# Kernel tuning notes

Measured on AMD Instinct MI355X. Metric: run time of the kernel, lower is better.

Reference implementation:

```python
import jax, jax.numpy as jnp
import numpy as np
from math import sqrt

ALPHA = 1.0
EPS = 1e-8


def setup_inputs() -> dict:
    key = jax.random.key(0)
    k1, k2, k3 = jax.random.split(key, 3)
    B, L, S, H, E = 4, 2048, 2048, 16, 64
    queries = jax.random.normal(k1, (B, L, H, E), dtype=jnp.float32)
    keys = jax.random.normal(k2, (B, S, H, E), dtype=jnp.float32)
    values = jax.random.normal(k3, (B, S, H, E), dtype=jnp.float32)
    return {"queries": queries, "keys": keys, "values": values}


def reference(queries, keys, values):
    B, L, H, E = queries.shape
    scale = 1.0 / sqrt(E)
    # dot product scores: [B,H,L,S]
    dot = jnp.einsum('blhe,bshe->bhls', queries, keys)
    # squared norms: [B,H,L,1] and [B,H,1,S]
    qn2 = jnp.sum(queries * queries, axis=-1).transpose(0, 2, 1)[..., :, None]
    kn2 = jnp.sum(keys * keys, axis=-1).transpose(0, 2, 1)[..., None, :]
    # wedge (parallelogram area) norm^2 = |q|^2|k|^2 - (q.k)^2, clipped at 0
    wedge_norm = jnp.sqrt(jax.nn.relu(qn2 * kn2 - dot * dot) + EPS)
    scores = ((1.0 - ALPHA) * dot + ALPHA * wedge_norm) * scale
    A = jax.nn.softmax(scores, axis=-1)  # no mask (mask_flag=False), dropout=0
    V = jnp.einsum('bhls,bshd->blhd', A, values)
    return V, jnp.mean(jnp.abs(scores))
```

## Files before the change

### kernel.cpp

```cpp
#include <hip/hip_runtime.h>
#include <math.h>

constexpr int Bb = 4, Ll = 2048, Ss = 2048, Hh = 16, Ee = 64;
constexpr float S2E  = 0.125f * 1.44269504088896341f;
constexpr float EPS2 = 1e-8f * S2E * S2E;
constexpr float INV_CNT = 1.0f / (4.0f * 16.0f * 2048.0f * 2048.0f);
constexpr float SUM_SCALE = INV_CNT * 0.69314718055994531f;

typedef __attribute__((ext_vector_type(8))) short  short8;
typedef __attribute__((ext_vector_type(4))) float  floatx4;

#define MFMA __builtin_amdgcn_mfma_f32_16x16x32_bf16

#define GLL(gp, lp_)                                                       \
  __builtin_amdgcn_global_load_lds(                                        \
      (const __attribute__((address_space(1))) unsigned int*)(gp),         \
      (__attribute__((address_space(3))) unsigned int*)(lp_), 16, 0, 0)

__device__ __forceinline__ unsigned bfrnd(float f) {
  unsigned u = __builtin_bit_cast(unsigned, f);
  return u + 0x7fffu + ((u >> 16) & 1u);
}
__device__ __forceinline__ float sq4(float4 v) {
  return v.x * v.x + v.y * v.y + v.z * v.z + v.w * v.w;
}
__device__ __forceinline__ float4 mul4(float4 v, float s) {
  float4 r; r.x = v.x * s; r.y = v.y * s; r.z = v.z * s; r.w = v.w * s;
  return r;
}
__device__ __forceinline__ short8 pack8(float4 x, float4 y) {
  union { short8 s; unsigned u[4]; } r;
  r.u[0] = __builtin_amdgcn_perm(bfrnd(x.y), bfrnd(x.x), 0x07060302u);
  r.u[1] = __builtin_amdgcn_perm(bfrnd(x.w), bfrnd(x.z), 0x07060302u);
  r.u[2] = __builtin_amdgcn_perm(bfrnd(y.y), bfrnd(y.x), 0x07060302u);
  r.u[3] = __builtin_amdgcn_perm(bfrnd(y.w), bfrnd(y.z), 0x07060302u);
  return r.s;
}

__global__ __launch_bounds__(256) void geom_pre_kernel(
    const float* __restrict__ Kg, const float* __restrict__ Vg,
    short* __restrict__ Kbf, short* __restrict__ Vtg,
    float* __restrict__ kn2g, float* __restrict__ sumg) {
  const int tid = threadIdx.x, bid = blockIdx.x;
  const int st = bid & 31, h = (bid >> 5) & 15, b = bid >> 9;
  const int s0 = st * 64, bh = b * 16 + h;
  if (bid == 0 && tid == 0) *sumg = 0.0f;

  const int r64 = tid >> 2, ec = (tid & 3) * 16;
  const float4* kp = (const float4*)(Kg + (((size_t)b * Ss + s0 + r64) * Hh + h) * Ee + ec);
  float4 k0 = kp[0], k1 = kp[1], k2 = kp[2], k3 = kp[3];
  float kn = sq4(k0) + sq4(k1) + sq4(k2) + sq4(k3);
  kn += __shfl_xor(kn, 1);
  kn += __shfl_xor(kn, 2);
  if ((tid & 3) == 0) kn2g[(size_t)bh * Ss + s0 + r64] = kn;
  short* ko = Kbf + ((size_t)bh * Ss + s0 + r64) * Ee + ec;
  *(short8*)(ko)     = pack8(k0, k1);
  *(short8*)(ko + 8) = pack8(k2, k3);

  const int sq = tid >> 4, eq = tid & 15;
  const float* vb = Vg + (((size_t)b * Ss + s0 + sq * 4) * Hh + h) * Ee + eq * 4;
  float4 r0 = *(const float4*)(vb);
  float4 r1 = *(const float4*)(vb + Hh * Ee);
  float4 r2 = *(const float4*)(vb + 2 * Hh * Ee);
  float4 r3 = *(const float4*)(vb + 3 * Hh * Ee);
  short* vo = Vtg + ((size_t)bh * Ee + eq * 4) * Ss + s0 + sq * 4;
#pragma unroll
  for (int j = 0; j < 4; ++j) {
    uint2 t;
    t.x = __builtin_amdgcn_perm(bfrnd((&r1.x)[j]), bfrnd((&r0.x)[j]), 0x07060302u);
    t.y = __builtin_amdgcn_perm(bfrnd((&r3.x)[j]), bfrnd((&r2.x)[j]), 0x07060302u);
    *(uint2*)(vo + (size_t)j * Ss) = t;
  }
}

constexpr int KB0 = 0, VB0 = 8192, PB = 16384, KN2 = 24576;

__global__ __launch_bounds__(256, 4) void geom_attn_kernel(
    const float* __restrict__ Qg, const short* __restrict__ Kbf,
    const short* __restrict__ Vtg, const float* __restrict__ kn2g,
    float* __restrict__ outg, float* __restrict__ sumg) {
  __shared__ __align__(16) char smem[32768];

  const int tid = threadIdx.x, w = tid >> 6, lane = tid & 63;
  const int c = lane & 15, q4 = lane >> 4;
  const int bid = blockIdx.x;
  const int lt = bid & 15, h = (bid >> 4) & 15, b = bid >> 8;
  const int bh = b * 16 + h;
  const int l0 = lt * 128 + w * 32;

  short8 qb[2][2];
  float qn2v[2];
#pragma unroll
  for (int g = 0; g < 2; ++g) {
    const float4* qp = (const float4*)(Qg + (((size_t)b * Ll + l0 + g * 16 + c) * Hh + h) * Ee);
    float4 a0 = mul4(qp[2 * q4], S2E),     a1 = mul4(qp[2 * q4 + 1], S2E);
    float4 a2 = mul4(qp[8 + 2 * q4], S2E), a3 = mul4(qp[9 + 2 * q4], S2E);
    float qn = sq4(a0) + sq4(a1) + sq4(a2) + sq4(a3);
    qn += __shfl_xor(qn, 16);
    qn += __shfl_xor(qn, 32);
    qn2v[g] = qn;
    qb[g][0] = pack8(a0, a1);
    qb[g][1] = pack8(a2, a3);
  }

  const int rK = tid >> 3, pK = tid & 7;
  const char* kSrc = (const char*)Kbf + (size_t)bh * (Ss * 128) + rK * 128 + ((pK ^ (rK & 7)) * 16);
  const int eV = tid >> 2;
  const char* vSrc = (const char*)Vtg + (size_t)bh * (Ss * 128) + eV * (Ss * 2) + (((tid & 3) ^ (eV & 3)) * 16);
  char* kDstW = smem + KB0 + w * 1024;
  char* vDstW = smem + VB0 + w * 1024;

  {
    const char* knSrc = (const char*)kn2g + (size_t)bh * 8192 + (size_t)tid * 16;
    GLL(knSrc, smem + KN2 + w * 1024);
    GLL(knSrc + 4096, smem + KN2 + w * 1024 + 4096);
  }

  GLL(kSrc, kDstW);
  GLL(vSrc, vDstW);
  kSrc += 4096;
  vSrc += 64;

  floatx4 o[2][4] = {};
  float lp0 = 0.f, lp1 = 0.f, scsum = 0.f;

  const int kOff = c * 128 + ((q4 ^ (c & 7)) * 16);
  const int vOff = c * 64 + ((q4 ^ (c & 3)) * 16);
  const int pRd  = PB + w * 2048 + c * 64 + ((q4 ^ (c & 3)) * 16);
  const int pWrB = PB + w * 2048 + c * 64 + (q4 & 1) * 8;
  const int knRd = KN2 + q4 * 16;

  for (int it = 0; it < 64; ++it) {
    const int p = it & 1;
    __syncthreads();
    GLL(kSrc, kDstW + (p ^ 1) * 4096);
    GLL(vSrc, vDstW + (p ^ 1) * 4096);
    kSrc += 4096;
    vSrc += 64;

    const char* Kb = smem + KB0 + p * 4096;
    const char* Vb = smem + VB0 + p * 4096;

#pragma unroll
    for (int ct = 0; ct < 2; ++ct) {
      short8 ka0 = *(const short8*)(Kb + ct * 2048 + kOff);
      short8 ka1 = *(const short8*)(Kb + ct * 2048 + (kOff ^ 64));
      float4 knv = *(const float4*)(smem + knRd + it * 128 + ct * 64);
      const int pwCT = ((ct * 2 + (q4 >> 1)) ^ (c & 3)) * 16;
#pragma unroll
      for (int g = 0; g < 2; ++g) {
        floatx4 d = {0.f, 0.f, 0.f, 0.f};
        d = MFMA(ka0, qb[g][0], d, 0, 0, 0);
        d = MFMA(ka1, qb[g][1], d, 0, 0, 0);
        float pe[4];
#pragma unroll
        for (int r = 0; r < 4; ++r) {
          float dot = d[r];
          float w2 = fmaf(-dot, dot, qn2v[g] * (&knv.x)[r]);
          w2 = fmaxf(w2, EPS2);
          float rt = __builtin_amdgcn_sqrtf(w2);
          scsum += rt;
          float e = __builtin_amdgcn_exp2f(rt);
          if (g == 0) lp0 += e; else lp1 += e;
          pe[r] = e;
        }
        uint2 pk;
        pk.x = __builtin_amdgcn_perm(__builtin_bit_cast(unsigned, pe[1]),
                                     __builtin_bit_cast(unsigned, pe[0]), 0x07060302u);
        pk.y = __builtin_amdgcn_perm(__builtin_bit_cast(unsigned, pe[3]),
                                     __builtin_bit_cast(unsigned, pe[2]), 0x07060302u);
        *(uint2*)(smem + pWrB + g * 1024 + pwCT) = pk;
      }
    }

    short8 vb0 = *(const short8*)(Vb + vOff);
    short8 vb1 = *(const short8*)(Vb + 1024 + vOff);
    short8 vb2 = *(const short8*)(Vb + 2048 + vOff);
    short8 vb3 = *(const short8*)(Vb + 3072 + vOff);
#pragma unroll
    for (int g = 0; g < 2; ++g) {
      short8 pa = *(const short8*)(smem + pRd + g * 1024);
      o[g][0] = MFMA(pa, vb0, o[g][0], 0, 0, 0);
      o[g][1] = MFMA(pa, vb1, o[g][1], 0, 0, 0);
      o[g][2] = MFMA(pa, vb2, o[g][2], 0, 0, 0);
      o[g][3] = MFMA(pa, vb3, o[g][3], 0, 0, 0);
    }
  }

  __syncthreads();

  lp0 += __shfl_xor(lp0, 16); lp0 += __shfl_xor(lp0, 32);
  lp1 += __shfl_xor(lp1, 16); lp1 += __shfl_xor(lp1, 32);

#pragma unroll
  for (int g = 0; g < 2; ++g) {
    float lpg = (g == 0) ? lp0 : lp1;
#pragma unroll
    for (int r = 0; r < 4; ++r) {
      float inv = 1.0f / __shfl(lpg, q4 * 4 + r);
      float* orow = outg + (((size_t)b * Ll + l0 + g * 16 + q4 * 4 + r) * Hh + h) * Ee;
      orow[c]      = o[g][0][r] * inv;
      orow[16 + c] = o[g][1][r] * inv;
      orow[32 + c] = o[g][2][r] * inv;
      orow[48 + c] = o[g][3][r] * inv;
    }
  }

  scsum += __shfl_xor(scsum, 1);
  scsum += __shfl_xor(scsum, 2);
  scsum += __shfl_xor(scsum, 4);
  scsum += __shfl_xor(scsum, 8);
  scsum += __shfl_xor(scsum, 16);
  scsum += __shfl_xor(scsum, 32);
  if (lane == 0) atomicAdd(sumg, scsum * SUM_SCALE);
}

extern "C" void kernel_launch(void* const* d_in, const int* in_sizes, int n_in,
                              void* d_out, int out_size, void* d_ws, size_t ws_size,
                              hipStream_t stream) {
  const float* Q = (const float*)d_in[0];
  const float* K = (const float*)d_in[1];
  const float* V = (const float*)d_in[2];
  float* out   = (float*)d_out;
  float* sumsc = out + (size_t)Bb * Ll * Hh * Ee;

  short* Kbf = (short*)d_ws;
  short* Vtg = Kbf + (size_t)Bb * Hh * Ss * Ee;
  float* kn2 = (float*)(Vtg + (size_t)Bb * Hh * Ee * Ss);

  hipLaunchKernelGGL(geom_pre_kernel, dim3(Bb * Hh * (Ss / 64)), dim3(256), 0,
                     stream, K, V, Kbf, Vtg, kn2, sumsc);
  hipLaunchKernelGGL(geom_attn_kernel, dim3(Bb * Hh * (Ll / 128)), dim3(256), 0,
                     stream, Q, Kbf, Vtg, kn2, out, sumsc);
}
```

Measured before the change: 267.5 us.

## Split attention block into eight waves of sixteen query rows each

```diff
diff --git a/kernel.cpp b/kernel.cpp
--- a/kernel.cpp
+++ b/kernel.cpp
@@ -75,7 +75,7 @@
 
 constexpr int KB0 = 0, VB0 = 8192, PB = 16384, KN2 = 24576;
 
-__global__ __launch_bounds__(256, 4) void geom_attn_kernel(
+__global__ __launch_bounds__(512, 8) void geom_attn_kernel(
     const float* __restrict__ Qg, const short* __restrict__ Kbf,
     const short* __restrict__ Vtg, const float* __restrict__ kn2g,
     float* __restrict__ outg, float* __restrict__ sumg) {
@@ -86,57 +86,58 @@
   const int bid = blockIdx.x;
   const int lt = bid & 15, h = (bid >> 4) & 15, b = bid >> 8;
   const int bh = b * 16 + h;
-  const int l0 = lt * 128 + w * 32;
-
-  short8 qb[2][2];
-  float qn2v[2];
-#pragma unroll
-  for (int g = 0; g < 2; ++g) {
-    const float4* qp = (const float4*)(Qg + (((size_t)b * Ll + l0 + g * 16 + c) * Hh + h) * Ee);
+  const int l0w = lt * 128 + w * 16;
+
+  short8 qb0, qb1;
+  float qn2v;
+  {
+    const float4* qp = (const float4*)(Qg + (((size_t)b * Ll + l0w + c) * Hh + h) * Ee);
     float4 a0 = mul4(qp[2 * q4], S2E),     a1 = mul4(qp[2 * q4 + 1], S2E);
     float4 a2 = mul4(qp[8 + 2 * q4], S2E), a3 = mul4(qp[9 + 2 * q4], S2E);
     float qn = sq4(a0) + sq4(a1) + sq4(a2) + sq4(a3);
     qn += __shfl_xor(qn, 16);
     qn += __shfl_xor(qn, 32);
-    qn2v[g] = qn;
-    qb[g][0] = pack8(a0, a1);
-    qb[g][1] = pack8(a2, a3);
-  }
-
-  const int rK = tid >> 3, pK = tid & 7;
-  const char* kSrc = (const char*)Kbf + (size_t)bh * (Ss * 128) + rK * 128 + ((pK ^ (rK & 7)) * 16);
-  const int eV = tid >> 2;
-  const char* vSrc = (const char*)Vtg + (size_t)bh * (Ss * 128) + eV * (Ss * 2) + (((tid & 3) ^ (eV & 3)) * 16);
-  char* kDstW = smem + KB0 + w * 1024;
-  char* vDstW = smem + VB0 + w * 1024;
-
-  {
-    const char* knSrc = (const char*)kn2g + (size_t)bh * 8192 + (size_t)tid * 16;
-    GLL(knSrc, smem + KN2 + w * 1024);
-    GLL(knSrc + 4096, smem + KN2 + w * 1024 + 4096);
-  }
-
-  GLL(kSrc, kDstW);
-  GLL(vSrc, vDstW);
-  kSrc += 4096;
-  vSrc += 64;
-
-  floatx4 o[2][4] = {};
-  float lp0 = 0.f, lp1 = 0.f, scsum = 0.f;
+    qn2v = qn;
+    qb0 = pack8(a0, a1);
+    qb1 = pack8(a2, a3);
+  }
+
+  const char* gSrc;
+  char* gDst;
+  int gStep;
+  if (w < 4) {
+    const int vt = w * 64 + lane;
+    const int rK = vt >> 3, pK = vt & 7;
+    gSrc = (const char*)Kbf + (size_t)bh * (Ss * 128) + rK * 128 + ((pK ^ (rK & 7)) * 16);
+    gDst = smem + KB0 + w * 1024;
+    gStep = 4096;
+  } else {
+    const int vt = (w - 4) * 64 + lane;
+    const int eV = vt >> 2;
+    gSrc = (const char*)Vtg + (size_t)bh * (Ss * 128) + eV * (Ss * 2) + (((vt & 3) ^ (eV & 3)) * 16);
+    gDst = smem + VB0 + (w - 4) * 1024;
+    gStep = 64;
+  }
+
+  GLL((const char*)kn2g + (size_t)bh * 8192 + (size_t)tid * 16, smem + KN2 + w * 1024);
+
+  GLL(gSrc, gDst);
+  gSrc += gStep;
+
+  floatx4 o[4] = {};
+  float lp = 0.f, scsum = 0.f;
 
   const int kOff = c * 128 + ((q4 ^ (c & 7)) * 16);
   const int vOff = c * 64 + ((q4 ^ (c & 3)) * 16);
-  const int pRd  = PB + w * 2048 + c * 64 + ((q4 ^ (c & 3)) * 16);
-  const int pWrB = PB + w * 2048 + c * 64 + (q4 & 1) * 8;
+  const int pRd  = PB + w * 1024 + c * 64 + ((q4 ^ (c & 3)) * 16);
+  const int pWrB = PB + w * 1024 + c * 64 + (q4 & 1) * 8;
   const int knRd = KN2 + q4 * 16;
 
   for (int it = 0; it < 64; ++it) {
     const int p = it & 1;
     __syncthreads();
-    GLL(kSrc, kDstW + (p ^ 1) * 4096);
-    GLL(vSrc, vDstW + (p ^ 1) * 4096);
-    kSrc += 4096;
-    vSrc += 64;
+    GLL(gSrc, gDst + (p ^ 1) * 4096);
+    gSrc += gStep;
 
     const char* Kb = smem + KB0 + p * 4096;
     const char* Vb = smem + VB0 + p * 4096;
@@ -147,63 +148,53 @@
       short8 ka1 = *(const short8*)(Kb + ct * 2048 + (kOff ^ 64));
       float4 knv = *(const float4*)(smem + knRd + it * 128 + ct * 64);
       const int pwCT = ((ct * 2 + (q4 >> 1)) ^ (c & 3)) * 16;
-#pragma unroll
-      for (int g = 0; g < 2; ++g) {
-        floatx4 d = {0.f, 0.f, 0.f, 0.f};
-        d = MFMA(ka0, qb[g][0], d, 0, 0, 0);
-        d = MFMA(ka1, qb[g][1], d, 0, 0, 0);
-        float pe[4];
-#pragma unroll
-        for (int r = 0; r < 4; ++r) {
-          float dot = d[r];
-          float w2 = fmaf(-dot, dot, qn2v[g] * (&knv.x)[r]);
-          w2 = fmaxf(w2, EPS2);
-          float rt = __builtin_amdgcn_sqrtf(w2);
-          scsum += rt;
-          float e = __builtin_amdgcn_exp2f(rt);
-          if (g == 0) lp0 += e; else lp1 += e;
-          pe[r] = e;
-        }
-        uint2 pk;
-        pk.x = __builtin_amdgcn_perm(__builtin_bit_cast(unsigned, pe[1]),
-                                     __builtin_bit_cast(unsigned, pe[0]), 0x07060302u);
-        pk.y = __builtin_amdgcn_perm(__builtin_bit_cast(unsigned, pe[3]),
-                                     __builtin_bit_cast(unsigned, pe[2]), 0x07060302u);
-        *(uint2*)(smem + pWrB + g * 1024 + pwCT) = pk;
+      floatx4 d = {0.f, 0.f, 0.f, 0.f};
+      d = MFMA(ka0, qb0, d, 0, 0, 0);
+      d = MFMA(ka1, qb1, d, 0, 0, 0);
+      float pe[4];
+#pragma unroll
+      for (int r = 0; r < 4; ++r) {
+        float dot = d[r];
+        float w2 = fmaf(-dot, dot, qn2v * (&knv.x)[r]);
+        w2 = fmaxf(w2, EPS2);
+        float rt = __builtin_amdgcn_sqrtf(w2);
+        scsum += rt;
+        float e = __builtin_amdgcn_exp2f(rt);
+        lp += e;
+        pe[r] = e;
       }
+      uint2 pk;
+      pk.x = __builtin_amdgcn_perm(__builtin_bit_cast(unsigned, pe[1]),
+                                   __builtin_bit_cast(unsigned, pe[0]), 0x07060302u);
+      pk.y = __builtin_amdgcn_perm(__builtin_bit_cast(unsigned, pe[3]),
+                                   __builtin_bit_cast(unsigned, pe[2]), 0x07060302u);
+      *(uint2*)(smem + pWrB + pwCT) = pk;
     }
 
     short8 vb0 = *(const short8*)(Vb + vOff);
     short8 vb1 = *(const short8*)(Vb + 1024 + vOff);
     short8 vb2 = *(const short8*)(Vb + 2048 + vOff);
     short8 vb3 = *(const short8*)(Vb + 3072 + vOff);
-#pragma unroll
-    for (int g = 0; g < 2; ++g) {
-      short8 pa = *(const short8*)(smem + pRd + g * 1024);
-      o[g][0] = MFMA(pa, vb0, o[g][0], 0, 0, 0);
-      o[g][1] = MFMA(pa, vb1, o[g][1], 0, 0, 0);
-      o[g][2] = MFMA(pa, vb2, o[g][2], 0, 0, 0);
-      o[g][3] = MFMA(pa, vb3, o[g][3], 0, 0, 0);
-    }
+    short8 pa = *(const short8*)(smem + pRd);
+    o[0] = MFMA(pa, vb0, o[0], 0, 0, 0);
+    o[1] = MFMA(pa, vb1, o[1], 0, 0, 0);
+    o[2] = MFMA(pa, vb2, o[2], 0, 0, 0);
+    o[3] = MFMA(pa, vb3, o[3], 0, 0, 0);
   }
 
   __syncthreads();
 
-  lp0 += __shfl_xor(lp0, 16); lp0 += __shfl_xor(lp0, 32);
-  lp1 += __shfl_xor(lp1, 16); lp1 += __shfl_xor(lp1, 32);
-
-#pragma unroll
-  for (int g = 0; g < 2; ++g) {
-    float lpg = (g == 0) ? lp0 : lp1;
-#pragma unroll
-    for (int r = 0; r < 4; ++r) {
-      float inv = 1.0f / __shfl(lpg, q4 * 4 + r);
-      float* orow = outg + (((size_t)b * Ll + l0 + g * 16 + q4 * 4 + r) * Hh + h) * Ee;
-      orow[c]      = o[g][0][r] * inv;
-      orow[16 + c] = o[g][1][r] * inv;
-      orow[32 + c] = o[g][2][r] * inv;
-      orow[48 + c] = o[g][3][r] * inv;
-    }
+  lp += __shfl_xor(lp, 16);
+  lp += __shfl_xor(lp, 32);
+
+#pragma unroll
+  for (int r = 0; r < 4; ++r) {
+    float inv = 1.0f / __shfl(lp, q4 * 4 + r);
+    float* orow = outg + (((size_t)b * Ll + l0w + q4 * 4 + r) * Hh + h) * Ee;
+    orow[c]      = o[0][r] * inv;
+    orow[16 + c] = o[1][r] * inv;
+    orow[32 + c] = o[2][r] * inv;
+    orow[48 + c] = o[3][r] * inv;
   }
 
   scsum += __shfl_xor(scsum, 1);
@@ -230,6 +221,6 @@
 
   hipLaunchKernelGGL(geom_pre_kernel, dim3(Bb * Hh * (Ss / 64)), dim3(256), 0,
                      stream, K, V, Kbf, Vtg, kn2, sumsc);
-  hipLaunchKernelGGL(geom_attn_kernel, dim3(Bb * Hh * (Ll / 128)), dim3(256), 0,
+  hipLaunchKernelGGL(geom_attn_kernel, dim3(Bb * Hh * (Ll / 128)), dim3(512), 0,
                      stream, Q, Kbf, Vtg, kn2, out, sumsc);
 }
```

New measurement: 315.0 us. 1.18x slower.

## Switch attention to 32x32x16 MFMA and pass P through permlane swaps

Applied to the files above, without the earlier changes.

```diff
diff --git a/kernel.cpp b/kernel.cpp
--- a/kernel.cpp
+++ b/kernel.cpp
@@ -7,10 +7,11 @@
 constexpr float INV_CNT = 1.0f / (4.0f * 16.0f * 2048.0f * 2048.0f);
 constexpr float SUM_SCALE = INV_CNT * 0.69314718055994531f;
 
-typedef __attribute__((ext_vector_type(8))) short  short8;
-typedef __attribute__((ext_vector_type(4))) float  floatx4;
-
-#define MFMA __builtin_amdgcn_mfma_f32_16x16x32_bf16
+typedef __attribute__((ext_vector_type(8)))  short short8;
+typedef __attribute__((ext_vector_type(4)))  float floatx4;
+typedef __attribute__((ext_vector_type(16))) float floatx16;
+
+#define MFMA32 __builtin_amdgcn_mfma_f32_32x32x16_bf16
 
 #define GLL(gp, lp_)                                                       \
   __builtin_amdgcn_global_load_lds(                                        \
@@ -35,6 +36,9 @@
   r.u[2] = __builtin_amdgcn_perm(bfrnd(y.y), bfrnd(y.x), 0x07060302u);
   r.u[3] = __builtin_amdgcn_perm(bfrnd(y.w), bfrnd(y.z), 0x07060302u);
   return r.s;
+}
+__device__ __forceinline__ void pl32swap(unsigned &a, unsigned &b) {
+  asm("v_permlane32_swap_b32 %0, %1" : "+v"(a), "+v"(b));
 }
 
 __global__ __launch_bounds__(256) void geom_pre_kernel(
@@ -73,34 +77,35 @@
   }
 }
 
-constexpr int KB0 = 0, VB0 = 8192, PB = 16384, KN2 = 24576;
+constexpr int KB0 = 0, VB0 = 8192, KN2 = 16384;
 
 __global__ __launch_bounds__(256, 4) void geom_attn_kernel(
     const float* __restrict__ Qg, const short* __restrict__ Kbf,
     const short* __restrict__ Vtg, const float* __restrict__ kn2g,
     float* __restrict__ outg, float* __restrict__ sumg) {
-  __shared__ __align__(16) char smem[32768];
+  __shared__ __align__(16) char smem[24576];
 
   const int tid = threadIdx.x, w = tid >> 6, lane = tid & 63;
-  const int c = lane & 15, q4 = lane >> 4;
+  const int l31 = lane & 31, hi = lane >> 5;
   const int bid = blockIdx.x;
   const int lt = bid & 15, h = (bid >> 4) & 15, b = bid >> 8;
   const int bh = b * 16 + h;
-  const int l0 = lt * 128 + w * 32;
-
-  short8 qb[2][2];
-  float qn2v[2];
-#pragma unroll
-  for (int g = 0; g < 2; ++g) {
-    const float4* qp = (const float4*)(Qg + (((size_t)b * Ll + l0 + g * 16 + c) * Hh + h) * Ee);
-    float4 a0 = mul4(qp[2 * q4], S2E),     a1 = mul4(qp[2 * q4 + 1], S2E);
-    float4 a2 = mul4(qp[8 + 2 * q4], S2E), a3 = mul4(qp[9 + 2 * q4], S2E);
-    float qn = sq4(a0) + sq4(a1) + sq4(a2) + sq4(a3);
-    qn += __shfl_xor(qn, 16);
+  const int l0w = lt * 128 + w * 32;
+
+  short8 qB[4];
+  float qn2v;
+  {
+    const float* qrow = Qg + (((size_t)b * Ll + l0w + l31) * Hh + h) * Ee;
+    float qn = 0.f;
+#pragma unroll
+    for (int ks = 0; ks < 4; ++ks) {
+      float4 a0 = mul4(*(const float4*)(qrow + ks * 16 + hi * 8), S2E);
+      float4 a1 = mul4(*(const float4*)(qrow + ks * 16 + hi * 8 + 4), S2E);
+      qn += sq4(a0) + sq4(a1);
+      qB[ks] = pack8(a0, a1);
+    }
     qn += __shfl_xor(qn, 32);
-    qn2v[g] = qn;
-    qb[g][0] = pack8(a0, a1);
-    qb[g][1] = pack8(a2, a3);
+    qn2v = qn;
   }
 
   const int rK = tid >> 3, pK = tid & 7;
@@ -121,14 +126,11 @@
   kSrc += 4096;
   vSrc += 64;
 
-  floatx4 o[2][4] = {};
-  float lp0 = 0.f, lp1 = 0.f, scsum = 0.f;
-
-  const int kOff = c * 128 + ((q4 ^ (c & 7)) * 16);
-  const int vOff = c * 64 + ((q4 ^ (c & 3)) * 16);
-  const int pRd  = PB + w * 2048 + c * 64 + ((q4 ^ (c & 3)) * 16);
-  const int pWrB = PB + w * 2048 + c * 64 + (q4 & 1) * 8;
-  const int knRd = KN2 + q4 * 16;
+  floatx16 o[2] = {};
+  float lp = 0.f, scsum = 0.f;
+
+  const int kSwz = l31 & 7;
+  const int vSwz = l31 & 3;
 
   for (int it = 0; it < 64; ++it) {
     const int p = it & 1;
@@ -141,69 +143,74 @@
     const char* Kb = smem + KB0 + p * 4096;
     const char* Vb = smem + VB0 + p * 4096;
 
-#pragma unroll
-    for (int ct = 0; ct < 2; ++ct) {
-      short8 ka0 = *(const short8*)(Kb + ct * 2048 + kOff);
-      short8 ka1 = *(const short8*)(Kb + ct * 2048 + (kOff ^ 64));
-      float4 knv = *(const float4*)(smem + knRd + it * 128 + ct * 64);
-      const int pwCT = ((ct * 2 + (q4 >> 1)) ^ (c & 3)) * 16;
-#pragma unroll
-      for (int g = 0; g < 2; ++g) {
-        floatx4 d = {0.f, 0.f, 0.f, 0.f};
-        d = MFMA(ka0, qb[g][0], d, 0, 0, 0);
-        d = MFMA(ka1, qb[g][1], d, 0, 0, 0);
-        float pe[4];
-#pragma unroll
-        for (int r = 0; r < 4; ++r) {
-          float dot = d[r];
-          float w2 = fmaf(-dot, dot, qn2v[g] * (&knv.x)[r]);
-          w2 = fmaxf(w2, EPS2);
-          float rt = __builtin_amdgcn_sqrtf(w2);
-          scsum += rt;
-          float e = __builtin_amdgcn_exp2f(rt);
-          if (g == 0) lp0 += e; else lp1 += e;
-          pe[r] = e;
-        }
-        uint2 pk;
-        pk.x = __builtin_amdgcn_perm(__builtin_bit_cast(unsigned, pe[1]),
-                                     __builtin_bit_cast(unsigned, pe[0]), 0x07060302u);
-        pk.y = __builtin_amdgcn_perm(__builtin_bit_cast(unsigned, pe[3]),
-                                     __builtin_bit_cast(unsigned, pe[2]), 0x07060302u);
-        *(uint2*)(smem + pWrB + g * 1024 + pwCT) = pk;
+    short8 ka0 = *(const short8*)(Kb + l31 * 128 + (((0 + hi) ^ kSwz) * 16));
+    short8 ka1 = *(const short8*)(Kb + l31 * 128 + (((2 + hi) ^ kSwz) * 16));
+    short8 ka2 = *(const short8*)(Kb + l31 * 128 + (((4 + hi) ^ kSwz) * 16));
+    short8 ka3 = *(const short8*)(Kb + l31 * 128 + (((6 + hi) ^ kSwz) * 16));
+    floatx16 d = {};
+    d = MFMA32(ka0, qB[0], d, 0, 0, 0);
+    d = MFMA32(ka1, qB[1], d, 0, 0, 0);
+    d = MFMA32(ka2, qB[2], d, 0, 0, 0);
+    d = MFMA32(ka3, qB[3], d, 0, 0, 0);
+
+    short8 vb00 = *(const short8*)(Vb + l31 * 64 + (((0 + hi) ^ vSwz) * 16));
+    short8 vb01 = *(const short8*)(Vb + l31 * 64 + (((2 + hi) ^ vSwz) * 16));
+    short8 vb10 = *(const short8*)(Vb + (32 + l31) * 64 + (((0 + hi) ^ vSwz) * 16));
+    short8 vb11 = *(const short8*)(Vb + (32 + l31) * 64 + (((2 + hi) ^ vSwz) * 16));
+
+    float4 knv0 = *(const float4*)(smem + KN2 + it * 128 + 0 * 32 + hi * 16);
+    float4 knv1 = *(const float4*)(smem + KN2 + it * 128 + 1 * 32 + hi * 16);
+    float4 knv2 = *(const float4*)(smem + KN2 + it * 128 + 2 * 32 + hi * 16);
+    float4 knv3 = *(const float4*)(smem + KN2 + it * 128 + 3 * 32 + hi * 16);
+
+    unsigned pk[4][2];
+#pragma unroll
+    for (int q = 0; q < 4; ++q) {
+      const float4 knq = (q == 0) ? knv0 : (q == 1) ? knv1 : (q == 2) ? knv2 : knv3;
+      float pe[4];
+#pragma unroll
+      for (int r = 0; r < 4; ++r) {
+        float dot = d[4 * q + r];
+        float w2 = fmaf(-dot, dot, qn2v * (&knq.x)[r]);
+        w2 = fmaxf(w2, EPS2);
+        float rt = __builtin_amdgcn_sqrtf(w2);
+        scsum += rt;
+        float e = __builtin_amdgcn_exp2f(rt);
+        lp += e;
+        pe[r] = e;
       }
+      pk[q][0] = __builtin_amdgcn_perm(__builtin_bit_cast(unsigned, pe[1]),
+                                       __builtin_bit_cast(unsigned, pe[0]), 0x07060302u);
+      pk[q][1] = __builtin_amdgcn_perm(__builtin_bit_cast(unsigned, pe[3]),
+                                       __builtin_bit_cast(unsigned, pe[2]), 0x07060302u);
     }
 
-    short8 vb0 = *(const short8*)(Vb + vOff);
-    short8 vb1 = *(const short8*)(Vb + 1024 + vOff);
-    short8 vb2 = *(const short8*)(Vb + 2048 + vOff);
-    short8 vb3 = *(const short8*)(Vb + 3072 + vOff);
-#pragma unroll
-    for (int g = 0; g < 2; ++g) {
-      short8 pa = *(const short8*)(smem + pRd + g * 1024);
-      o[g][0] = MFMA(pa, vb0, o[g][0], 0, 0, 0);
-      o[g][1] = MFMA(pa, vb1, o[g][1], 0, 0, 0);
-      o[g][2] = MFMA(pa, vb2, o[g][2], 0, 0, 0);
-      o[g][3] = MFMA(pa, vb3, o[g][3], 0, 0, 0);
-    }
+    pl32swap(pk[0][0], pk[1][0]);
+    pl32swap(pk[0][1], pk[1][1]);
+    pl32swap(pk[2][0], pk[3][0]);
+    pl32swap(pk[2][1], pk[3][1]);
+    union { unsigned u[4]; short8 s; } pa0, pa1;
+    pa0.u[0] = pk[0][0]; pa0.u[1] = pk[0][1]; pa0.u[2] = pk[1][0]; pa0.u[3] = pk[1][1];
+    pa1.u[0] = pk[2][0]; pa1.u[1] = pk[2][1]; pa1.u[2] = pk[3][0]; pa1.u[3] = pk[3][1];
+
+    o[0] = MFMA32(pa0.s, vb00, o[0], 0, 0, 0);
+    o[0] = MFMA32(pa1.s, vb01, o[0], 0, 0, 0);
+    o[1] = MFMA32(pa0.s, vb10, o[1], 0, 0, 0);
+    o[1] = MFMA32(pa1.s, vb11, o[1], 0, 0, 0);
   }
 
   __syncthreads();
 
-  lp0 += __shfl_xor(lp0, 16); lp0 += __shfl_xor(lp0, 32);
-  lp1 += __shfl_xor(lp1, 16); lp1 += __shfl_xor(lp1, 32);
-
-#pragma unroll
-  for (int g = 0; g < 2; ++g) {
-    float lpg = (g == 0) ? lp0 : lp1;
-#pragma unroll
-    for (int r = 0; r < 4; ++r) {
-      float inv = 1.0f / __shfl(lpg, q4 * 4 + r);
-      float* orow = outg + (((size_t)b * Ll + l0 + g * 16 + q4 * 4 + r) * Hh + h) * Ee;
-      orow[c]      = o[g][0][r] * inv;
-      orow[16 + c] = o[g][1][r] * inv;
-      orow[32 + c] = o[g][2][r] * inv;
-      orow[48 + c] = o[g][3][r] * inv;
-    }
+  lp += __shfl_xor(lp, 32);
+  float lpinv = 1.0f / lp;
+
+#pragma unroll
+  for (int r = 0; r < 16; ++r) {
+    const int row = (r & 3) + 8 * (r >> 2) + 4 * hi;
+    float inv = __shfl(lpinv, row);
+    float* orow = outg + (((size_t)b * Ll + l0w + row) * Hh + h) * Ee + l31;
+    orow[0]  = o[0][r] * inv;
+    orow[32] = o[1][r] * inv;
   }
 
   scsum += __shfl_xor(scsum, 1);
```

Result: faster. 259.3 us (-3.1%).
